# Optimization experiments

Measured on AMD Instinct MI355X. Metric: run time of the kernel, lower is better.

The kernel has to match this reference:

```python
import jax, jax.numpy as jnp
import numpy as np

B, L, C, H, K = 2, 2048, 1024, 16, 32
Dh = C // H


def setup_inputs() -> dict:
    key = jax.random.key(0)
    ks = jax.random.split(key, 6)
    x = jax.random.normal(ks[0], (B, L, C), dtype=jnp.float32)
    # indices: self index first, then K-1 random neighbors (shared across batch & heads)
    self_idx = jnp.arange(L, dtype=jnp.int32).reshape(1, L, 1)
    rand_idx = jax.random.randint(ks[1], (1, L, K - 1), 0, L, dtype=jnp.int32)
    idx = jnp.concatenate([self_idx, rand_idx], axis=-1)  # (1, L, K)
    s = 1.0 / np.sqrt(C)
    Wq = jax.random.normal(ks[2], (C, C), dtype=jnp.float32) * s
    Wk = jax.random.normal(ks[3], (C, C), dtype=jnp.float32) * s
    Wv = jax.random.normal(ks[4], (C, C), dtype=jnp.float32) * s
    Wo = jax.random.normal(ks[5], (C, C), dtype=jnp.float32) * s
    return {"x": x, "idx": idx, "Wq": Wq, "Wk": Wk, "Wv": Wv, "Wo": Wo}


def reference(x, idx, Wq, Wk, Wv, Wo):
    # projections (torch Linear: y = x @ W.T), reshape to (B, H, L, Dh)
    def heads(y):
        return y.reshape(B, L, H, Dh).transpose(0, 2, 1, 3)

    q = heads(x @ Wq.T)
    k = heads(x @ Wk.T)
    v = heads(x @ Wv.T)

    idx0 = idx[0]  # (L, K) shared across batch and heads
    k_n = jnp.take(k, idx0, axis=2)  # (B, H, L, K, Dh)
    v_n = jnp.take(v, idx0, axis=2)  # (B, H, L, K, Dh)

    q = q / jnp.sqrt(jnp.asarray(Dh, q.dtype))
    attn = jnp.einsum("bhld,bhlkd->bhlk", q, k_n)
    attn = jax.nn.softmax(attn, axis=-1)
    out = jnp.einsum("bhlk,bhlkd->bhld", attn, v_n)
    out = out.transpose(0, 2, 1, 3).reshape(B, L, C)
    return out @ Wo.T
```

## Files before the change

kernel.cpp:

```cpp
#include <hip/hip_runtime.h>
#include <hip/hip_bf16.h>

#define B_  2
#define L_  2048
#define C_  1024
#define H_  16
#define K_  32
#define DH_ 64
#define M_  (B_ * L_)

typedef __hip_bfloat16 bf16;
typedef __attribute__((ext_vector_type(4))) float f32x4;
typedef __attribute__((ext_vector_type(8))) short short8;
typedef __attribute__((ext_vector_type(8))) unsigned short u16x8;

__device__ inline unsigned short f2bf(float f) {
    __hip_bfloat16 h = __float2bfloat16(f);
    return *reinterpret_cast<unsigned short*>(&h);
}
__device__ inline float bf2f(unsigned short u) {
    return __uint_as_float(((unsigned)u) << 16);
}
__device__ inline void gld_lds16(const bf16* g, bf16* l) {
    __builtin_amdgcn_global_load_lds(
        (const __attribute__((address_space(1))) void*)g,
        (__attribute__((address_space(3))) void*)l,
        16, 0, 0);
}

__global__ void __launch_bounds__(256) cvt_all(
    const float* __restrict__ x,  const float* __restrict__ wq,
    const float* __restrict__ wk, const float* __restrict__ wv,
    const float* __restrict__ wo,
    bf16* __restrict__ xb,  bf16* __restrict__ wqb, bf16* __restrict__ wkb,
    bf16* __restrict__ wvb, bf16* __restrict__ wob)
{
    int g = blockIdx.x * 256 + threadIdx.x;
    const float* src; bf16* dst; int o;
    if (g < 1048576)      { src = x;  dst = xb;  o = g; }
    else if (g < 1310720) { src = wq; dst = wqb; o = g - 1048576; }
    else if (g < 1572864) { src = wk; dst = wkb; o = g - 1310720; }
    else if (g < 1835008) { src = wv; dst = wvb; o = g - 1572864; }
    else                  { src = wo; dst = wob; o = g - 1835008; }
    float4 f = reinterpret_cast<const float4*>(src)[o];
    ushort4 u;
    u.x = f2bf(f.x); u.y = f2bf(f.y); u.z = f2bf(f.z); u.w = f2bf(f.w);
    reinterpret_cast<ushort4*>(dst)[o] = u;
}

struct GemmArgs {
    const bf16* A;
    const bf16* W[3];
    bf16* Yb[3];
    float scale0;
};

__global__ void __launch_bounds__(256) gemm_qkv(GemmArgs ga)
{
    __shared__ bf16 As[128 * 64];
    __shared__ bf16 Bs[128 * 64];

    const int m0  = blockIdx.x * 128;
    const int nt  = blockIdx.y;
    const int seg = nt >> 3;
    const int n0  = (nt & 7) * 128;
    const bf16* __restrict__ A = ga.A;
    const bf16* __restrict__ W = ga.W[seg];
    const float scale = (seg == 0) ? ga.scale0 : 1.0f;

    const int t    = threadIdx.x;
    const int lane = t & 63;
    const int w    = t >> 6;
    const int wm   = w >> 1;
    const int wn   = w & 1;

    const int subrow = lane >> 3;
    const int kc     = lane & 7;

    f32x4 acc[4][4] = {};

    for (int kt = 0; kt < 16; ++kt) {
        const int k0 = kt * 64;
        if (kt) __syncthreads();
        #pragma unroll
        for (int i = 0; i < 4; ++i) {
            const int r0  = w * 32 + i * 8;
            const int row = r0 + subrow;
            const int kcs = kc ^ (subrow & 7);
            gld_lds16(A + (size_t)(m0 + row) * 1024 + k0 + kcs * 8, As + r0 * 64);
        }
        #pragma unroll
        for (int i = 0; i < 4; ++i) {
            const int r0  = w * 32 + i * 8;
            const int row = r0 + subrow;
            const int kcs = kc ^ (subrow & 7);
            gld_lds16(W + (size_t)(n0 + row) * 1024 + k0 + kcs * 8, Bs + r0 * 64);
        }
        __syncthreads();
        #pragma unroll
        for (int ks = 0; ks < 2; ++ks) {
            short8 af[4], bfv[4];
            #pragma unroll
            for (int mf = 0; mf < 4; ++mf) {
                const int row    = wm * 64 + mf * 16 + (lane & 15);
                const int kchunk = ks * 4 + (lane >> 4);
                const int pc     = kchunk ^ (row & 7);
                af[mf] = *reinterpret_cast<const short8*>(As + row * 64 + pc * 8);
            }
            #pragma unroll
            for (int nf = 0; nf < 4; ++nf) {
                const int row    = wn * 64 + nf * 16 + (lane & 15);
                const int kchunk = ks * 4 + (lane >> 4);
                const int pc     = kchunk ^ (row & 7);
                bfv[nf] = *reinterpret_cast<const short8*>(Bs + row * 64 + pc * 8);
            }
            #pragma unroll
            for (int mf = 0; mf < 4; ++mf)
                #pragma unroll
                for (int nf = 0; nf < 4; ++nf)
                    acc[mf][nf] = __builtin_amdgcn_mfma_f32_16x16x32_bf16(
                        af[mf], bfv[nf], acc[mf][nf], 0, 0, 0);
        }
    }

    #pragma unroll
    for (int mf = 0; mf < 4; ++mf) {
        #pragma unroll
        for (int nf = 0; nf < 4; ++nf) {
            const int row = m0 + wm * 64 + mf * 16 + ((lane >> 4) << 2);
            const int col = n0 + wn * 64 + nf * 16 + (lane & 15);
            #pragma unroll
            for (int r = 0; r < 4; ++r)
                ga.Yb[seg][(size_t)(row + r) * 1024 + col] =
                    __float2bfloat16(acc[mf][nf][r] * scale);
        }
    }
}

__global__ void __launch_bounds__(256) gemm_out(
    const bf16* __restrict__ A, const bf16* __restrict__ W,
    float* __restrict__ Yf)
{
    __shared__ bf16 As[128 * 64];
    __shared__ bf16 Bs[64 * 64];

    const int m0 = blockIdx.x * 128;
    const int n0 = blockIdx.y * 64;

    const int t    = threadIdx.x;
    const int lane = t & 63;
    const int w    = t >> 6;
    const int wm   = w >> 1;
    const int wn   = w & 1;

    const int subrow = lane >> 3;
    const int kc     = lane & 7;

    f32x4 acc[4][2] = {};

    for (int kt = 0; kt < 16; ++kt) {
        const int k0 = kt * 64;
        if (kt) __syncthreads();
        #pragma unroll
        for (int i = 0; i < 4; ++i) {
            const int r0  = w * 32 + i * 8;
            const int row = r0 + subrow;
            const int kcs = kc ^ (subrow & 7);
            gld_lds16(A + (size_t)(m0 + row) * 1024 + k0 + kcs * 8, As + r0 * 64);
        }
        #pragma unroll
        for (int i = 0; i < 2; ++i) {
            const int r0  = w * 16 + i * 8;
            const int row = r0 + subrow;
            const int kcs = kc ^ (subrow & 7);
            gld_lds16(W + (size_t)(n0 + row) * 1024 + k0 + kcs * 8, Bs + r0 * 64);
        }
        __syncthreads();
        #pragma unroll
        for (int ks = 0; ks < 2; ++ks) {
            short8 af[4], bfv[2];
            #pragma unroll
            for (int mf = 0; mf < 4; ++mf) {
                const int row    = wm * 64 + mf * 16 + (lane & 15);
                const int kchunk = ks * 4 + (lane >> 4);
                const int pc     = kchunk ^ (row & 7);
                af[mf] = *reinterpret_cast<const short8*>(As + row * 64 + pc * 8);
            }
            #pragma unroll
            for (int nf = 0; nf < 2; ++nf) {
                const int row    = wn * 32 + nf * 16 + (lane & 15);
                const int kchunk = ks * 4 + (lane >> 4);
                const int pc     = kchunk ^ (row & 7);
                bfv[nf] = *reinterpret_cast<const short8*>(Bs + row * 64 + pc * 8);
            }
            #pragma unroll
            for (int mf = 0; mf < 4; ++mf)
                #pragma unroll
                for (int nf = 0; nf < 2; ++nf)
                    acc[mf][nf] = __builtin_amdgcn_mfma_f32_16x16x32_bf16(
                        af[mf], bfv[nf], acc[mf][nf], 0, 0, 0);
        }
    }

    #pragma unroll
    for (int mf = 0; mf < 4; ++mf) {
        #pragma unroll
        for (int nf = 0; nf < 2; ++nf) {
            const int row = m0 + wm * 64 + mf * 16 + ((lane >> 4) << 2);
            const int col = n0 + wn * 32 + nf * 16 + (lane & 15);
            #pragma unroll
            for (int r = 0; r < 4; ++r)
                Yf[(size_t)(row + r) * 1024 + col] = acc[mf][nf][r];
        }
    }
}

__global__ void __launch_bounds__(256) attn_knn(
    const bf16* __restrict__ qg, const bf16* __restrict__ kg,
    const bf16* __restrict__ vg, const int* __restrict__ idx,
    bf16* __restrict__ ao)
{
    const int slot = blockIdx.x;
    const int b    = slot >> 2;
    const int wg   = slot & 3;
    const int l    = blockIdx.y * 4 + (threadIdx.x >> 6);

    const int lane = threadIdx.x & 63;
    const int hw   = lane >> 4;
    const int h    = wg * 4 + hw;
    const int sl   = lane & 15;
    const int half = sl >> 3;
    const int c8   = sl & 7;

    const size_t rowq = (size_t)b * L_ + l;
    const unsigned short* kg16 = reinterpret_cast<const unsigned short*>(kg);
    const unsigned short* vg16 = reinterpret_cast<const unsigned short*>(vg);
    const size_t hoff = (size_t)h * DH_ + c8 * 8;

    int4 iv[4];
    #pragma unroll
    for (int i = 0; i < 4; ++i)
        iv[i] = reinterpret_cast<const int4*>(idx + l * K_ + half * 16)[i];

    u16x8 qv = *reinterpret_cast<const u16x8*>(
        reinterpret_cast<const unsigned short*>(qg) + rowq * C_ + hoff);
    float qf[8];
    #pragma unroll
    for (int e = 0; e < 8; ++e) qf[e] = bf2f(qv[e]);

    float s[16];
    #pragma unroll
    for (int jj = 0; jj < 16; ++jj) {
        const int4 q4 = iv[jj >> 2];
        const int row = (jj & 3) == 0 ? q4.x : (jj & 3) == 1 ? q4.y
                       : (jj & 3) == 2 ? q4.z : q4.w;
        const u16x8 kv = *reinterpret_cast<const u16x8*>(
            kg16 + ((size_t)b * L_ + row) * C_ + hoff);
        float acc = 0.f;
        #pragma unroll
        for (int e = 0; e < 8; ++e) acc += qf[e] * bf2f(kv[e]);
        s[jj] = acc;
    }

    #pragma unroll
    for (int jj = 0; jj < 16; ++jj) {
        float x = s[jj];
        x += __shfl_xor(x, 1, 16);
        x += __shfl_xor(x, 2, 16);
        x += __shfl_xor(x, 4, 16);
        s[jj] = x;
    }

    float m = s[0];
    #pragma unroll
    for (int jj = 1; jj < 16; ++jj) m = fmaxf(m, s[jj]);
    m = fmaxf(m, __shfl_xor(m, 8, 16));
    float ssum = 0.f;
    #pragma unroll
    for (int jj = 0; jj < 16; ++jj) { s[jj] = __expf(s[jj] - m); ssum += s[jj]; }
    ssum += __shfl_xor(ssum, 8, 16);
    const float inv = 1.0f / ssum;

    float acc[8] = {0.f, 0.f, 0.f, 0.f, 0.f, 0.f, 0.f, 0.f};
    #pragma unroll
    for (int jj = 0; jj < 16; ++jj) {
        const int4 q4 = iv[jj >> 2];
        const int row = (jj & 3) == 0 ? q4.x : (jj & 3) == 1 ? q4.y
                       : (jj & 3) == 2 ? q4.z : q4.w;
        const u16x8 vv = *reinterpret_cast<const u16x8*>(
            vg16 + ((size_t)b * L_ + row) * C_ + hoff);
        const float p = s[jj];
        #pragma unroll
        for (int e = 0; e < 8; ++e) acc[e] += p * bf2f(vv[e]);
    }
    #pragma unroll
    for (int e = 0; e < 8; ++e) acc[e] += __shfl_xor(acc[e], 8, 16);

    if (half == 0) {
        u16x8 o;
        #pragma unroll
        for (int e = 0; e < 8; ++e) o[e] = f2bf(acc[e] * inv);
        *reinterpret_cast<u16x8*>(ao + rowq * C_ + hoff) = o;
    }
}

extern "C" void kernel_launch(void* const* d_in, const int* in_sizes, int n_in,
                              void* d_out, int out_size, void* d_ws, size_t ws_size,
                              hipStream_t stream)
{
    const float* x  = (const float*)d_in[0];
    const int*   idx = (const int*)d_in[1];
    const float* Wq = (const float*)d_in[2];
    const float* Wk = (const float*)d_in[3];
    const float* Wv = (const float*)d_in[4];
    const float* Wo = (const float*)d_in[5];
    float* out = (float*)d_out;

    char* ws = (char*)d_ws;
    bf16* xb  = (bf16*)(ws + 0);
    bf16* wqb = (bf16*)(ws + 8388608);
    bf16* wkb = (bf16*)(ws + 10485760);
    bf16* wvb = (bf16*)(ws + 12582912);
    bf16* wob = (bf16*)(ws + 14680064);
    bf16* qb  = (bf16*)(ws + 16777216);
    bf16* kb  = (bf16*)(ws + 25165824);
    bf16* vb  = (bf16*)(ws + 33554432);
    bf16* ab  = (bf16*)(ws + 41943040);

    cvt_all<<<8192, 256, 0, stream>>>(x, Wq, Wk, Wv, Wo, xb, wqb, wkb, wvb, wob);

    GemmArgs g1;
    g1.A = xb;
    g1.W[0] = wqb; g1.W[1] = wkb; g1.W[2] = wvb;
    g1.Yb[0] = qb; g1.Yb[1] = kb; g1.Yb[2] = vb;
    g1.scale0 = 0.125f;
    gemm_qkv<<<dim3(32, 24), 256, 0, stream>>>(g1);

    attn_knn<<<dim3(8, 512), 256, 0, stream>>>(qb, kb, vb, idx, ab);

    gemm_out<<<dim3(32, 16), 256, 0, stream>>>(ab, wob, out);
}
```

Measured before the change: 85.67 us.

## Rewrite QKV GEMM with 256x256 tiles and double-buffered LDS pipeline

Replaces the 128x128 QKV projection GEMM with a 512-thread kernel that computes 256x256 output tiles. It stages tiles into a 128KB double-buffered LDS area, split into half-tiles, with explicit vmcnt waits and barriers so the next K-step's loads overlap the MFMA work. It also remaps block IDs into groups to improve L2 reuse, and raises wave priority around the MFMA bursts. The larger tiles cut global and LDS traffic per FLOP. The cost is only 192 workgroups with one block per CU, which may leave part of the GPU idle, plus much higher register and LDS pressure.

```diff
diff --git a/kernel.cpp b/kernel.cpp
--- a/kernel.cpp
+++ b/kernel.cpp
@@ -48,91 +48,131 @@
     reinterpret_cast<ushort4*>(dst)[o] = u;
 }
 
-struct GemmArgs {
+struct Gemm8Args {
     const bf16* A;
     const bf16* W[3];
-    bf16* Yb[3];
+    bf16* Y[3];
     float scale0;
 };
 
-__global__ void __launch_bounds__(256) gemm_qkv(GemmArgs ga)
-{
-    __shared__ bf16 As[128 * 64];
-    __shared__ bf16 Bs[128 * 64];
-
-    const int m0  = blockIdx.x * 128;
-    const int nt  = blockIdx.y;
-    const int seg = nt >> 3;
-    const int n0  = (nt & 7) * 128;
+#define STGH(bufn, ht, Gptr, rbase, kt) {                                    \
+    _Pragma("unroll")                                                        \
+    for (int i_ = 0; i_ < 2; ++i_) {                                         \
+        const int row_ = i_ * 64 + w * 8 + (lane >> 3);                      \
+        const int ch_  = (lane & 7) ^ (row_ & 7);                            \
+        gld_lds16((Gptr) + (size_t)((rbase) + row_) * 1024 + (kt) * 64 + ch_ * 8, \
+                  smb + (size_t)(bufn) * 32768 + (ht) * 8192                 \
+                      + (i_ * 64 + w * 8) * 64);                             \
+    }                                                                        \
+}
+
+#define RDA(bufn, ah, ks) {                                                  \
+    _Pragma("unroll")                                                        \
+    for (int mf = 0; mf < 8; ++mf) {                                         \
+        const int r_ = mf * 16 + (lane & 15);                                \
+        const int c_ = ((ks) * 4 + (lane >> 4)) ^ (r_ & 7);                  \
+        ak[mf] = *reinterpret_cast<const short8*>(                           \
+            smb + (size_t)(bufn) * 32768 + (ah) * 8192 + r_ * 64 + c_ * 8);  \
+    }                                                                        \
+}
+
+#define RDB(bufn, ks) {                                                      \
+    _Pragma("unroll")                                                        \
+    for (int nf = 0; nf < 2; ++nf) {                                         \
+        const int c_col = wn * 32 + nf * 16 + (lane & 15);                   \
+        const int bh_   = 1 + (c_col >> 7);                                  \
+        const int r_    = c_col & 127;                                       \
+        const int c_    = ((ks) * 4 + (lane >> 4)) ^ (r_ & 7);               \
+        bk[nf] = *reinterpret_cast<const short8*>(                           \
+            smb + (size_t)(bufn) * 32768 + bh_ * 8192 + r_ * 64 + c_ * 8);   \
+    }                                                                        \
+}
+
+#define MAC(p) {                                                             \
+    __builtin_amdgcn_s_setprio(1);                                           \
+    _Pragma("unroll")                                                        \
+    for (int mf = 0; mf < 8; ++mf)                                           \
+        _Pragma("unroll")                                                    \
+        for (int nf = 0; nf < 2; ++nf)                                       \
+            acc[p][mf][nf] = __builtin_amdgcn_mfma_f32_16x16x32_bf16(        \
+                ak[mf], bk[nf], acc[p][mf][nf], 0, 0, 0);                    \
+    __builtin_amdgcn_s_setprio(0);                                           \
+}
+
+__global__ void __launch_bounds__(512, 1) gemm8_qkv(Gemm8Args ga)
+{
+    extern __shared__ __align__(16) char smraw[];
+    bf16* smb = (bf16*)smraw;
+
+    const int bid = blockIdx.x;
+    const int nid = (bid & 7) * 24 + (bid >> 3);
+    const int bm  = nid & 15;
+    const int bn  = nid >> 4;
+    const int m0  = bm * 256;
+    const int seg = bn >> 2;
+    const int nw0 = (bn & 3) * 256;
+
     const bf16* __restrict__ A = ga.A;
     const bf16* __restrict__ W = ga.W[seg];
+    bf16* __restrict__ Y = ga.Y[seg];
     const float scale = (seg == 0) ? ga.scale0 : 1.0f;
 
-    const int t    = threadIdx.x;
-    const int lane = t & 63;
-    const int w    = t >> 6;
-    const int wm   = w >> 1;
-    const int wn   = w & 1;
-
-    const int subrow = lane >> 3;
-    const int kc     = lane & 7;
-
-    f32x4 acc[4][4] = {};
-
-    for (int kt = 0; kt < 16; ++kt) {
-        const int k0 = kt * 64;
-        if (kt) __syncthreads();
-        #pragma unroll
-        for (int i = 0; i < 4; ++i) {
-            const int r0  = w * 32 + i * 8;
-            const int row = r0 + subrow;
-            const int kcs = kc ^ (subrow & 7);
-            gld_lds16(A + (size_t)(m0 + row) * 1024 + k0 + kcs * 8, As + r0 * 64);
-        }
-        #pragma unroll
-        for (int i = 0; i < 4; ++i) {
-            const int r0  = w * 32 + i * 8;
-            const int row = r0 + subrow;
-            const int kcs = kc ^ (subrow & 7);
-            gld_lds16(W + (size_t)(n0 + row) * 1024 + k0 + kcs * 8, Bs + r0 * 64);
-        }
-        __syncthreads();
-        #pragma unroll
-        for (int ks = 0; ks < 2; ++ks) {
-            short8 af[4], bfv[4];
-            #pragma unroll
-            for (int mf = 0; mf < 4; ++mf) {
-                const int row    = wm * 64 + mf * 16 + (lane & 15);
-                const int kchunk = ks * 4 + (lane >> 4);
-                const int pc     = kchunk ^ (row & 7);
-                af[mf] = *reinterpret_cast<const short8*>(As + row * 64 + pc * 8);
+    const int tid  = threadIdx.x;
+    const int lane = tid & 63;
+    const int w    = tid >> 6;
+    const int wn   = w;
+
+    f32x4 acc[2][8][2] = {};
+    short8 ak[8], bk[2];
+
+    STGH(0, 0, A, m0,        0);
+    STGH(0, 1, W, nw0,       0);
+    STGH(0, 2, W, nw0 + 128, 0);
+    STGH(0, 3, A, m0 + 128,  0);
+
+    #pragma unroll 1
+    for (int t = 0; t < 16; ++t) {
+        const int cur = t & 1;
+        const int nxt = cur ^ 1;
+        const bool more = (t < 15);
+
+        asm volatile("s_waitcnt vmcnt(2)" ::: "memory");
+        __builtin_amdgcn_s_barrier();
+        if (more) {
+            STGH(nxt, 0, A, m0,  t + 1);
+            STGH(nxt, 1, W, nw0, t + 1);
+        }
+        RDA(cur, 0, 0); RDB(cur, 0);
+        MAC(0);
+        RDA(cur, 0, 1); RDB(cur, 1);
+        MAC(0);
+
+        if (more) asm volatile("s_waitcnt vmcnt(4)" ::: "memory");
+        else      asm volatile("s_waitcnt vmcnt(0)" ::: "memory");
+        __builtin_amdgcn_s_barrier();
+        if (more) {
+            STGH(nxt, 2, W, nw0 + 128, t + 1);
+            STGH(nxt, 3, A, m0 + 128,  t + 1);
+        }
+        RDA(cur, 3, 0); RDB(cur, 0);
+        MAC(1);
+        RDA(cur, 3, 1); RDB(cur, 1);
+        MAC(1);
+    }
+
+    #pragma unroll
+    for (int p = 0; p < 2; ++p) {
+        #pragma unroll
+        for (int mf = 0; mf < 8; ++mf) {
+            #pragma unroll
+            for (int nf = 0; nf < 2; ++nf) {
+                const int row = m0 + p * 128 + mf * 16 + ((lane >> 4) << 2);
+                const int col = nw0 + wn * 32 + nf * 16 + (lane & 15);
+                #pragma unroll
+                for (int r = 0; r < 4; ++r)
+                    Y[(size_t)(row + r) * 1024 + col] =
+                        __float2bfloat16(acc[p][mf][nf][r] * scale);
             }
-            #pragma unroll
-            for (int nf = 0; nf < 4; ++nf) {
-                const int row    = wn * 64 + nf * 16 + (lane & 15);
-                const int kchunk = ks * 4 + (lane >> 4);
-                const int pc     = kchunk ^ (row & 7);
-                bfv[nf] = *reinterpret_cast<const short8*>(Bs + row * 64 + pc * 8);
-            }
-            #pragma unroll
-            for (int mf = 0; mf < 4; ++mf)
-                #pragma unroll
-                for (int nf = 0; nf < 4; ++nf)
-                    acc[mf][nf] = __builtin_amdgcn_mfma_f32_16x16x32_bf16(
-                        af[mf], bfv[nf], acc[mf][nf], 0, 0, 0);
-        }
-    }
-
-    #pragma unroll
-    for (int mf = 0; mf < 4; ++mf) {
-        #pragma unroll
-        for (int nf = 0; nf < 4; ++nf) {
-            const int row = m0 + wm * 64 + mf * 16 + ((lane >> 4) << 2);
-            const int col = n0 + wn * 64 + nf * 16 + (lane & 15);
-            #pragma unroll
-            for (int r = 0; r < 4; ++r)
-                ga.Yb[seg][(size_t)(row + r) * 1024 + col] =
-                    __float2bfloat16(acc[mf][nf][r] * scale);
         }
     }
 }
@@ -329,12 +369,12 @@
 
     cvt_all<<<8192, 256, 0, stream>>>(x, Wq, Wk, Wv, Wo, xb, wqb, wkb, wvb, wob);
 
-    GemmArgs g1;
+    Gemm8Args g1;
     g1.A = xb;
     g1.W[0] = wqb; g1.W[1] = wkb; g1.W[2] = wvb;
-    g1.Yb[0] = qb; g1.Yb[1] = kb; g1.Yb[2] = vb;
+    g1.Y[0] = qb;  g1.Y[1] = kb;  g1.Y[2] = vb;
     g1.scale0 = 0.125f;
-    gemm_qkv<<<dim3(32, 24), 256, 0, stream>>>(g1);
+    gemm8_qkv<<<192, 512, 131072, stream>>>(g1);
 
     attn_knn<<<dim3(8, 512), 256, 0, stream>>>(qb, kb, vb, idx, ab);
 
```

Result: slower. 92.19 us (+7.6%).
